# Kernel optimization log

Measured on AMD Instinct MI355X. Metric: run time of the kernel, lower is better.

## Reference

```python
import jax, jax.numpy as jnp
import numpy as np

N = 50000      # nodes
E = 800000     # edges
F_IN = 9       # node features
H = 128        # model_units
G = 64         # graphs in batch


def _lin_init(key, fan_in, fan_out):
    k1, k2 = jax.random.split(key)
    lim = 1.0 / np.sqrt(fan_in)
    W = jax.random.uniform(k1, (fan_in, fan_out), minval=-lim, maxval=lim, dtype=jnp.float32)
    b = jax.random.uniform(k2, (fan_out,), minval=-lim, maxval=lim, dtype=jnp.float32)
    return W, b


def setup_inputs() -> dict:
    key = jax.random.key(0)
    ks = jax.random.split(key, 12)
    x = jax.random.normal(ks[0], (N, F_IN), dtype=jnp.float32)
    edge_index = jax.random.randint(ks[1], (2, E), 0, N, dtype=jnp.int32)
    batch = jnp.sort(jax.random.randint(ks[2], (N,), 0, G, dtype=jnp.int32))
    W1, b1 = _lin_init(ks[3], F_IN, H)      # conv1 (GCN)
    W2, b2 = _lin_init(ks[4], H, H)         # conv2 (GCN, shared across layers)
    We1, be1 = _lin_init(ks[5], 2 * H, H)   # EdgeConv MLP layer 1
    We2, be2 = _lin_init(ks[6], H, H)       # EdgeConv MLP layer 2
    Wf1, bf1 = _lin_init(ks[7], H, H)
    Wf2, bf2 = _lin_init(ks[8], H, 32)
    Wf3, bf3 = _lin_init(ks[9], 32, 1)
    return {"x": x, "edge_index": edge_index, "batch": batch,
            "W1": W1, "b1": b1, "W2": W2, "b2": b2,
            "We1": We1, "be1": be1, "We2": We2, "be2": be2,
            "Wf1": Wf1, "bf1": bf1, "Wf2": Wf2, "bf2": bf2,
            "Wf3": Wf3, "bf3": bf3}


def _gcn(x, W, b, src, dst, dis):
    # GCNConv with implicit self-loops and symmetric normalization.
    h = x @ W                                              # [N,H]
    msg = h[src] * dis[src, None]                          # gather + scale
    agg = jax.ops.segment_sum(msg, dst, num_segments=N)    # scatter-add
    return dis[:, None] * agg + h * (dis * dis)[:, None] + b


def _edgeconv(x, We1, be1, We2, be2, src, dst):
    # EdgeConv: max_j MLP([x_i, x_j - x_i]) over incoming edges j->i.
    xi = x[dst]                                            # [E,H]
    xj = x[src]
    m = jnp.concatenate([xi, xj - xi], axis=-1)            # [E,2H]
    m = jax.nn.relu(m @ We1 + be1) @ We2 + be2             # [E,H]
    agg = jax.ops.segment_max(m, dst, num_segments=N)
    return jnp.where(jnp.isfinite(agg), agg, 0.0)          # isolated nodes -> 0


def reference(x, edge_index, batch, W1, b1, W2, b2, We1, be1, We2, be2,
              Wf1, bf1, Wf2, bf2, Wf3, bf3):
    src, dst = edge_index[0], edge_index[1]
    # degree (with self loop) for GCN normalization
    deg = jax.ops.segment_sum(jnp.ones((E,), jnp.float32), dst, num_segments=N) + 1.0
    dis = jax.lax.rsqrt(deg)

    h = jnp.tanh(_gcn(x, W1, b1, src, dst, dis))
    h = jnp.tanh(_edgeconv(h, We1, be1, We2, be2, src, dst))
    # model_layers = 3 -> loop body once, then final block (dropout = identity, eval)
    for _ in range(2):
        h = jnp.tanh(_gcn(h, W2, b2, src, dst, dis))
        h = jnp.tanh(_edgeconv(h, We1, be1, We2, be2, src, dst))

    h = jnp.tanh(h @ Wf1 + bf1)
    h = jnp.tanh(h @ Wf2 + bf2)
    h = h @ Wf3 + bf3                                      # [N,1]

    counts = jax.ops.segment_sum(jnp.ones((N,), jnp.float32), batch, num_segments=G)
    pooled = jax.ops.segment_sum(h, batch, num_segments=G) / jnp.maximum(counts, 1.0)[:, None]
    return jax.nn.sigmoid(pooled)                          # [G,1]
```

## Files before the change

### kernel.cpp

```cpp
#include <hip/hip_runtime.h>
#include <hip/hip_bf16.h>

#define N_NODES 50000
#define N_EDGES 800000
#define F_IN 9
#define H 128
#define G_GRAPHS 64
#define HH (H * H)
#define MAXT (N_EDGES / 16 + N_NODES)

typedef short bf16x8 __attribute__((ext_vector_type(8)));
typedef float f32x4 __attribute__((ext_vector_type(4)));
typedef float f32x2 __attribute__((ext_vector_type(2)));

static __device__ inline short f2b(float f) {
    __hip_bfloat16 h = __float2bfloat16(f);
    return *reinterpret_cast<short*>(&h);
}
static __device__ inline float blo(unsigned u) { return __uint_as_float(u << 16); }
static __device__ inline float bhi(unsigned u) { return __uint_as_float(u & 0xFFFF0000u); }
static __device__ inline f32x2 up2(unsigned u) {
    f32x2 r; r.x = __uint_as_float(u << 16); r.y = __uint_as_float(u); return r;
}
static __device__ inline unsigned encodef(float f) {
    unsigned u = __float_as_uint(f);
    return (u & 0x80000000u) ? ~u : (u | 0x80000000u);
}
static __device__ inline float decodef(unsigned u) {
    return __uint_as_float((u & 0x80000000u) ? (u ^ 0x80000000u) : ~u);
}
static __device__ inline unsigned cvtpk(float lo, float hi) {
    unsigned r;
    asm("v_cvt_pk_bf16_f32 %0, %1, %2" : "=v"(r) : "v"(lo), "v"(hi));
    return r;
}

__global__ __launch_bounds__(256) void k_detect(const unsigned* __restrict__ x, int* flag,
                                                float* pooled, float* counts) {
    __shared__ int cnt;
    if (threadIdx.x == 0) cnt = 0;
    __syncthreads();
    unsigned u = x[threadIdx.x];
    int e = (u >> 7) & 0xFF;
    if (e >= 0x70 && e <= 0x83) atomicAdd(&cnt, 1);
    if (threadIdx.x < G_GRAPHS) { pooled[threadIdx.x] = 0.f; counts[threadIdx.x] = 0.f; }
    __syncthreads();
    if (threadIdx.x == 0) *flag = (cnt >= 128) ? 1 : 0;
}

struct CvtArgs { const void* src[15]; float* dst[15]; };

__global__ __launch_bounds__(256) void k_cvt_all(CvtArgs a, const int* __restrict__ flag) {
    const int sz[15] = {450000, 1152, 128, 16384, 128, 32768, 128, 16384, 128,
                        16384, 128, 4096, 32, 32, 1};
    int i = blockIdx.x * 256 + threadIdx.x;
    int fl = *flag;
    int base = 0;
    #pragma unroll
    for (int s = 0; s < 15; ++s) {
        if (i >= base && i < base + sz[s]) {
            int off = i - base;
            float v = fl ? __bfloat162float(((const __hip_bfloat16*)a.src[s])[off])
                         : ((const float*)a.src[s])[off];
            a.dst[s][off] = v;
        }
        base += sz[s];
    }
}

__global__ __launch_bounds__(256) void k_zero(float* p, int n) {
    int i = blockIdx.x * 256 + threadIdx.x;
    if (i < n) p[i] = 0.f;
}

__global__ __launch_bounds__(256) void k_prep_all(const float* __restrict__ We1,
                                                  const float* __restrict__ W2,
                                                  const float* __restrict__ Wf1,
                                                  const float* __restrict__ Wf2,
                                                  const float* __restrict__ We2,
                                                  short* WfU, short* WfV, short* WfW2,
                                                  short* WfF1, short* WfF2, short* We2f) {
    int b = blockIdx.x;
    const float* W; const float* Wm = nullptr; short* out; int NT = 8; int tid;
    if (b < 8)       { W = We1;      Wm = We1 + HH; out = WfU;  tid = b * 256 + threadIdx.x; }
    else if (b < 16) { W = We1 + HH; out = WfV;  tid = (b - 8) * 256 + threadIdx.x; }
    else if (b < 24) { W = W2;       out = WfW2; tid = (b - 16) * 256 + threadIdx.x; }
    else if (b < 32) { W = Wf1;      out = WfF1; tid = (b - 24) * 256 + threadIdx.x; }
    else if (b < 40) { W = We2;      out = We2f; tid = (b - 32) * 256 + threadIdx.x; }
    else             { W = Wf2;      out = WfF2; NT = 2; tid = (b - 40) * 256 + threadIdx.x; }
    int total = 4 * NT * 64;
    if (tid >= total) return;
    int kc = tid / (NT * 64);
    int ct = (tid / 64) % NT;
    int lane = tid & 63;
    int Nc = NT * 16;
    int kb = kc * 32 + (lane >> 4) * 8;
    int col = ct * 16 + (lane & 15);
    #pragma unroll
    for (int j = 0; j < 8; ++j) {
        float w = W[(kb + j) * Nc + col];
        if (Wm) w -= Wm[(kb + j) * Nc + col];
        out[tid * 8 + j] = f2b(w);
    }
}

__global__ __launch_bounds__(256) void k_hist(const int* __restrict__ dst, int* cnt) {
    int e = blockIdx.x * 256 + threadIdx.x;
    if (e < N_EDGES) atomicAdd(&cnt[dst[e]], 1);
}

__global__ __launch_bounds__(256) void k_scan1d(const int* __restrict__ deg,
                                                int* __restrict__ outA, int* __restrict__ outB,
                                                int* __restrict__ bsA, int* __restrict__ bsB) {
    __shared__ int ldsA[256], ldsB[256];
    int base = blockIdx.x * 2048;
    int t = threadIdx.x;
    int localA[8], localB[8];
    int sA = 0, sB = 0;
    #pragma unroll
    for (int j = 0; j < 8; ++j) {
        int idx = base + t * 8 + j;
        int v = (idx < N_NODES) ? deg[idx] : 0;
        int tc = (v + 15) >> 4;
        localA[j] = sA; sA += v;
        localB[j] = sB; sB += tc;
    }
    ldsA[t] = sA; ldsB[t] = sB;
    __syncthreads();
    if (t == 0) {
        int run = 0;
        for (int i = 0; i < 256; ++i) { int v = ldsA[i]; ldsA[i] = run; run += v; }
        bsA[blockIdx.x] = run;
        run = 0;
        for (int i = 0; i < 256; ++i) { int v = ldsB[i]; ldsB[i] = run; run += v; }
        bsB[blockIdx.x] = run;
    }
    __syncthreads();
    int oA = ldsA[t], oB = ldsB[t];
    #pragma unroll
    for (int j = 0; j < 8; ++j) {
        int idx = base + t * 8 + j;
        if (idx < N_NODES) { outA[idx] = oA + localA[j]; outB[idx] = oB + localB[j]; }
    }
}

__global__ void k_scan2d(int* bsA, int* bsB, int nb, int* rowptr, int* tstart, int* ntiles) {
    int run = 0;
    for (int i = 0; i < nb; ++i) { int v = bsA[i]; bsA[i] = run; run += v; }
    rowptr[N_NODES] = N_EDGES;
    run = 0;
    for (int i = 0; i < nb; ++i) { int v = bsB[i]; bsB[i] = run; run += v; }
    tstart[N_NODES] = run;
    *ntiles = run;
}

__global__ __launch_bounds__(256) void k_scan3d(int* rowptr, int* tstart,
                                                const int* __restrict__ bsA,
                                                const int* __restrict__ bsB) {
    int idx = blockIdx.x * 256 + threadIdx.x;
    if (idx < N_NODES) {
        rowptr[idx] += bsA[idx >> 11];
        tstart[idx] += bsB[idx >> 11];
    }
}

__global__ __launch_bounds__(256) void k_scatter(const int* __restrict__ src, const int* __restrict__ dst,
                                                 const int* __restrict__ rowptr, int* cursor,
                                                 int* __restrict__ csr_src) {
    int e = blockIdx.x * 256 + threadIdx.x;
    if (e >= N_EDGES) return;
    int d = dst[e];
    int pos = rowptr[d] + atomicSub(&cursor[d], 1) - 1;
    csr_src[pos] = src[e];
}

__global__ __launch_bounds__(256) void k_dis_counts(const int* __restrict__ rowptr, float* dis,
                                                    const int* __restrict__ batch, float* counts) {
    __shared__ float lc[G_GRAPHS];
    if (threadIdx.x < G_GRAPHS) lc[threadIdx.x] = 0.f;
    __syncthreads();
    int n = blockIdx.x * 256 + threadIdx.x;
    if (n < N_NODES) {
        int deg = rowptr[n + 1] - rowptr[n];
        dis[n] = rsqrtf((float)deg + 1.0f);
        atomicAdd(&lc[batch[n]], 1.0f);
    }
    __syncthreads();
    if (threadIdx.x < G_GRAPHS && lc[threadIdx.x] > 0.f)
        atomicAdd(&counts[threadIdx.x], lc[threadIdx.x]);
}

__global__ __launch_bounds__(256) void k_tfill(const int* __restrict__ rowptr,
                                               const int* __restrict__ csr_src,
                                               const int* __restrict__ tstart,
                                               int* __restrict__ tileN,
                                               int* __restrict__ tileSrc) {
    int n = blockIdx.x * 256 + threadIdx.x;
    if (n >= N_NODES) return;
    int t0 = tstart[n], t1 = tstart[n + 1];
    int beg = rowptr[n], end = rowptr[n + 1];
    for (int t = t0; t < t1; ++t) {
        tileN[t] = n;
        int tb = beg + (t - t0) * 16;
        #pragma unroll 4
        for (int j = 0; j < 16; ++j) {
            int ei = tb + j;
            tileSrc[t * 16 + j] = csr_src[ei < end ? ei : end - 1];
        }
    }
}

__global__ __launch_bounds__(256) void k_gemm_f32bf_scale(const float* __restrict__ A,
                                                          const float* __restrict__ W,
                                                          const float* __restrict__ dis,
                                                          short* __restrict__ out, int M) {
    __shared__ float w_lds[F_IN * H];
    for (int i = threadIdx.x; i < F_IN * H; i += 256) w_lds[i] = W[i];
    __syncthreads();
    int row = blockIdx.x * 8 + threadIdx.x / 32;
    int c4 = (threadIdx.x & 31) << 2;
    if (row >= M) return;
    const float* a = A + (size_t)row * F_IN;
    float acc0 = 0.f, acc1 = 0.f, acc2 = 0.f, acc3 = 0.f;
    #pragma unroll
    for (int k = 0; k < F_IN; ++k) {
        float av = a[k];
        float4 w = *reinterpret_cast<const float4*>(&w_lds[k * H + c4]);
        acc0 = fmaf(av, w.x, acc0);
        acc1 = fmaf(av, w.y, acc1);
        acc2 = fmaf(av, w.z, acc2);
        acc3 = fmaf(av, w.w, acc3);
    }
    float dv = dis[row];
    uint2 o = make_uint2(cvtpk(acc0 * dv, acc1 * dv), cvtpk(acc2 * dv, acc3 * dv));
    *reinterpret_cast<uint2*>(&out[(size_t)row * H + c4]) = o;
}

__global__ __launch_bounds__(512) void k_gemm_dual(const short* __restrict__ A,
                                                   const short* __restrict__ WfU,
                                                   const short* __restrict__ WfV,
                                                   const float* __restrict__ be1,
                                                   short* __restrict__ U,
                                                   short* __restrict__ V,
                                                   unsigned* __restrict__ aggEnc, int M) {
    __shared__ short wl[32768];
    for (int i = threadIdx.x * 8; i < 16384; i += 4096) {
        *reinterpret_cast<f32x4*>(&wl[i])         = *reinterpret_cast<const f32x4*>(&WfU[i]);
        *reinterpret_cast<f32x4*>(&wl[16384 + i]) = *reinterpret_cast<const f32x4*>(&WfV[i]);
    }
    {
        int r0 = blockIdx.x * 128;
        uint4* base = reinterpret_cast<uint4*>(aggEnc + (size_t)r0 * H);
        const uint4 z = make_uint4(0, 0, 0, 0);
        #pragma unroll
        for (int i = 0; i < 8; ++i) {
            int idx = threadIdx.x + i * 512;
            int row = r0 + (idx >> 5);
            if (row < M) base[idx] = z;
        }
    }
    __syncthreads();
    int wv = threadIdx.x >> 6, lane = threadIdx.x & 63;
    int er = lane & 15, kg = lane >> 4;
    int row0 = (blockIdx.x * 8 + wv) * 16;
    if (row0 >= M) return;
    bf16x8 af[4];
    #pragma unroll
    for (int kc = 0; kc < 4; ++kc)
        af[kc] = *reinterpret_cast<const bf16x8*>(&A[(size_t)(row0 + er) * H + kc * 32 + kg * 8]);
    const f32x4 vzero = {0.f, 0.f, 0.f, 0.f};
    f32x4 acc[8];
    #pragma unroll
    for (int ct = 0; ct < 8; ++ct) acc[ct] = vzero;
    #pragma unroll
    for (int kc = 0; kc < 4; ++kc)
        #pragma unroll
        for (int ct = 0; ct < 8; ++ct) {
            bf16x8 bf = *reinterpret_cast<const bf16x8*>(&wl[((kc * 8 + ct) * 64 + lane) * 8]);
            acc[ct] = __builtin_amdgcn_mfma_f32_16x16x32_bf16(af[kc], bf, acc[ct], 0, 0, 0);
        }
    #pragma unroll
    for (int ct = 0; ct < 8; ++ct) {
        int col = ct * 16 + er;
        float bv = be1[col];
        #pragma unroll
        for (int r = 0; r < 4; ++r)
            U[(size_t)(row0 + kg * 4 + r) * H + col] = f2b(acc[ct][r] + bv);
    }
    #pragma unroll
    for (int ct = 0; ct < 8; ++ct) acc[ct] = vzero;
    #pragma unroll
    for (int kc = 0; kc < 4; ++kc)
        #pragma unroll
        for (int ct = 0; ct < 8; ++ct) {
            bf16x8 bf = *reinterpret_cast<const bf16x8*>(&wl[16384 + ((kc * 8 + ct) * 64 + lane) * 8]);
            acc[ct] = __builtin_amdgcn_mfma_f32_16x16x32_bf16(af[kc], bf, acc[ct], 0, 0, 0);
        }
    #pragma unroll
    for (int ct = 0; ct < 8; ++ct) {
        int col = ct * 16 + er;
        #pragma unroll
        for (int r = 0; r < 4; ++r)
            V[(size_t)(row0 + kg * 4 + r) * H + col] = f2b(acc[ct][r]);
    }
}

__global__ __launch_bounds__(512) void k_gemm_scale_agg(const unsigned* __restrict__ aggEnc,
                                                        const float* __restrict__ be2,
                                                        const short* __restrict__ Wf,
                                                        const float* __restrict__ dis,
                                                        short* __restrict__ out, int M) {
    __shared__ short wl[16384];
    for (int i = threadIdx.x * 8; i < 16384; i += 4096)
        *reinterpret_cast<f32x4*>(&wl[i]) = *reinterpret_cast<const f32x4*>(&Wf[i]);
    __syncthreads();
    int wv = threadIdx.x >> 6, lane = threadIdx.x & 63;
    int er = lane & 15, kg = lane >> 4;
    int row0 = (blockIdx.x * 8 + wv) * 16;
    if (row0 >= M) return;
    bf16x8 af[4];
    #pragma unroll
    for (int kc = 0; kc < 4; ++kc) {
        int basec = kc * 32 + kg * 8;
        const unsigned* ap = &aggEnc[(size_t)(row0 + er) * H + basec];
        uint4 q0 = *reinterpret_cast<const uint4*>(ap);
        uint4 q1 = *reinterpret_cast<const uint4*>(ap + 4);
        float f0 = q0.x ? tanhf(decodef(q0.x) + be2[basec + 0]) : 0.f;
        float f1 = q0.y ? tanhf(decodef(q0.y) + be2[basec + 1]) : 0.f;
        float f2 = q0.z ? tanhf(decodef(q0.z) + be2[basec + 2]) : 0.f;
        float f3 = q0.w ? tanhf(decodef(q0.w) + be2[basec + 3]) : 0.f;
        float f4 = q1.x ? tanhf(decodef(q1.x) + be2[basec + 4]) : 0.f;
        float f5 = q1.y ? tanhf(decodef(q1.y) + be2[basec + 5]) : 0.f;
        float f6 = q1.z ? tanhf(decodef(q1.z) + be2[basec + 6]) : 0.f;
        float f7 = q1.w ? tanhf(decodef(q1.w) + be2[basec + 7]) : 0.f;
        union { unsigned u[4]; bf16x8 v; } A;
        A.u[0] = cvtpk(f0, f1); A.u[1] = cvtpk(f2, f3);
        A.u[2] = cvtpk(f4, f5); A.u[3] = cvtpk(f6, f7);
        af[kc] = A.v;
    }
    const f32x4 vzero = {0.f, 0.f, 0.f, 0.f};
    f32x4 acc[8];
    #pragma unroll
    for (int ct = 0; ct < 8; ++ct) acc[ct] = vzero;
    #pragma unroll
    for (int kc = 0; kc < 4; ++kc)
        #pragma unroll
        for (int ct = 0; ct < 8; ++ct) {
            bf16x8 bf = *reinterpret_cast<const bf16x8*>(&wl[((kc * 8 + ct) * 64 + lane) * 8]);
            acc[ct] = __builtin_amdgcn_mfma_f32_16x16x32_bf16(af[kc], bf, acc[ct], 0, 0, 0);
        }
    float dv[4];
    #pragma unroll
    for (int r = 0; r < 4; ++r) dv[r] = dis[row0 + kg * 4 + r];
    #pragma unroll
    for (int ct = 0; ct < 8; ++ct) {
        int col = ct * 16 + er;
        #pragma unroll
        for (int r = 0; r < 4; ++r)
            out[(size_t)(row0 + kg * 4 + r) * H + col] = f2b(acc[ct][r] * dv[r]);
    }
}

__global__ __launch_bounds__(256) void k_gcn_fused(const int* __restrict__ rowptr,
                                                   const int* __restrict__ csr_src,
                                                   const short* __restrict__ hWs,
                                                   const float* __restrict__ dis,
                                                   const float* __restrict__ bias,
                                                   short* __restrict__ out) {
    int wv = threadIdx.x >> 6, lane = threadIdx.x & 63;
    const unsigned* hw = (const unsigned*)hWs;
    const f32x2 z2 = {0.f, 0.f};
    for (int n = blockIdx.x * 4 + wv; n < N_NODES; n += gridDim.x * 4) {
        int beg = rowptr[n], end = rowptr[n + 1];
        f32x2 sa = z2, sb = z2, sc = z2, sd = z2;
        int e = beg;
        for (; e + 8 <= end; e += 8) {
            int s0 = csr_src[e],     s1 = csr_src[e + 1], s2 = csr_src[e + 2], s3 = csr_src[e + 3];
            int s4 = csr_src[e + 4], s5 = csr_src[e + 5], s6 = csr_src[e + 6], s7 = csr_src[e + 7];
            unsigned w0 = hw[(size_t)s0 * 64 + lane];
            unsigned w1 = hw[(size_t)s1 * 64 + lane];
            unsigned w2 = hw[(size_t)s2 * 64 + lane];
            unsigned w3 = hw[(size_t)s3 * 64 + lane];
            unsigned w4 = hw[(size_t)s4 * 64 + lane];
            unsigned w5 = hw[(size_t)s5 * 64 + lane];
            unsigned w6 = hw[(size_t)s6 * 64 + lane];
            unsigned w7 = hw[(size_t)s7 * 64 + lane];
            sa += up2(w0); sb += up2(w1); sc += up2(w2); sd += up2(w3);
            sa += up2(w4); sb += up2(w5); sc += up2(w6); sd += up2(w7);
        }
        for (; e + 4 <= end; e += 4) {
            int s0 = csr_src[e], s1 = csr_src[e + 1], s2 = csr_src[e + 2], s3 = csr_src[e + 3];
            unsigned w0 = hw[(size_t)s0 * 64 + lane];
            unsigned w1 = hw[(size_t)s1 * 64 + lane];
            unsigned w2 = hw[(size_t)s2 * 64 + lane];
            unsigned w3 = hw[(size_t)s3 * 64 + lane];
            sa += up2(w0); sb += up2(w1); sc += up2(w2); sd += up2(w3);
        }
        for (; e < end; ++e) sa += up2(hw[(size_t)csr_src[e] * 64 + lane]);
        f32x2 s = (sa + sb) + (sc + sd);
        float dn = dis[n];
        f32x2 wn2 = up2(hw[(size_t)n * 64 + lane]);
        float r0 = tanhf(dn * (s.x + wn2.x) + bias[lane * 2]);
        float r1 = tanhf(dn * (s.y + wn2.y) + bias[lane * 2 + 1]);
        *reinterpret_cast<unsigned*>(&out[(size_t)n * H + lane * 2]) = cvtpk(r0, r1);
    }
}

__global__ __launch_bounds__(512) void k_edge_tile(const int* __restrict__ tileN,
                                                   const int* __restrict__ tileSrc,
                                                   const int* __restrict__ ntilesp,
                                                   const short* __restrict__ U,
                                                   const short* __restrict__ V,
                                                   const short* __restrict__ We2f,
                                                   unsigned* aggEnc) {
    int nt = *ntilesp;
    if ((int)(blockIdx.x * 8) >= nt) return;
    __shared__ short wl[16384];
    for (int i = threadIdx.x * 8; i < 16384; i += 4096)
        *reinterpret_cast<f32x4*>(&wl[i]) = *reinterpret_cast<const f32x4*>(&We2f[i]);
    __syncthreads();
    int wv = threadIdx.x >> 6, lane = threadIdx.x & 63;
    int er = lane & 15, kg = lane >> 4, kseg = kg * 8;
    int tid = blockIdx.x * 8 + wv;
    if (tid >= nt) return;
    int n = tileN[tid];
    int s = tileSrc[tid * 16 + er];
    const f32x4 vzero = {0.f, 0.f, 0.f, 0.f};
    const f32x2 z2 = {0.f, 0.f};
    f32x4 acc[8];
    #pragma unroll
    for (int ct = 0; ct < 8; ++ct) acc[ct] = vzero;
    #pragma unroll
    for (int kc = 0; kc < 4; ++kc) {
        uint4 uu4 = *reinterpret_cast<const uint4*>(&U[(size_t)n * H + kc * 32 + kseg]);
        uint4 vv4 = *reinterpret_cast<const uint4*>(&V[(size_t)s * H + kc * 32 + kseg]);
        union { unsigned u[4]; bf16x8 v; } A;
        f32x2 t;
        t = __builtin_elementwise_max(up2(uu4.x) + up2(vv4.x), z2); A.u[0] = cvtpk(t.x, t.y);
        t = __builtin_elementwise_max(up2(uu4.y) + up2(vv4.y), z2); A.u[1] = cvtpk(t.x, t.y);
        t = __builtin_elementwise_max(up2(uu4.z) + up2(vv4.z), z2); A.u[2] = cvtpk(t.x, t.y);
        t = __builtin_elementwise_max(up2(uu4.w) + up2(vv4.w), z2); A.u[3] = cvtpk(t.x, t.y);
        #pragma unroll
        for (int ct = 0; ct < 8; ++ct) {
            bf16x8 bf = *reinterpret_cast<const bf16x8*>(&wl[((kc * 8 + ct) * 64 + lane) * 8]);
            acc[ct] = __builtin_amdgcn_mfma_f32_16x16x32_bf16(A.v, bf, acc[ct], 0, 0, 0);
        }
    }
    float cm[8];
    #pragma unroll
    for (int ct = 0; ct < 8; ++ct) {
        float v = fmaxf(fmaxf(fmaxf(acc[ct][0], acc[ct][1]), acc[ct][2]), acc[ct][3]);
        v = fmaxf(v, __shfl_xor(v, 16));
        v = fmaxf(v, __shfl_xor(v, 32));
        cm[ct] = v;
    }
    float vA, vB;
    if (kg == 0)      { vA = cm[0]; vB = cm[1]; }
    else if (kg == 1) { vA = cm[2]; vB = cm[3]; }
    else if (kg == 2) { vA = cm[4]; vB = cm[5]; }
    else              { vA = cm[6]; vB = cm[7]; }
    int colA = (kg * 2) * 16 + er;
    int colB = (kg * 2 + 1) * 16 + er;
    atomicMax(&aggEnc[(size_t)n * H + colA], encodef(vA));
    atomicMax(&aggEnc[(size_t)n * H + colB], encodef(vB));
}

__global__ __launch_bounds__(512) void k_final_mlp_agg(const unsigned* __restrict__ aggEnc,
                                                       const float* __restrict__ be2,
                                                       const short* __restrict__ WfF1,
                                                       const short* __restrict__ WfF2,
                                                       const float* __restrict__ bf1,
                                                       const float* __restrict__ bf2,
                                                       const float* __restrict__ Wf3,
                                                       const float* __restrict__ bf3,
                                                       const int* __restrict__ batch,
                                                       float* pooled, int M) {
    __shared__ short wl1[16384];
    __shared__ short wl2[4096];
    __shared__ short tb[8][2048];
    __shared__ float lp[G_GRAPHS];
    for (int i = threadIdx.x * 8; i < 16384; i += 4096)
        *reinterpret_cast<f32x4*>(&wl1[i]) = *reinterpret_cast<const f32x4*>(&WfF1[i]);
    {
        int i = threadIdx.x * 8;
        if (i < 4096)
            *reinterpret_cast<f32x4*>(&wl2[i]) = *reinterpret_cast<const f32x4*>(&WfF2[i]);
    }
    if (threadIdx.x < G_GRAPHS) lp[threadIdx.x] = 0.f;
    __syncthreads();
    int wv = threadIdx.x >> 6, lane = threadIdx.x & 63;
    int er = lane & 15, kg = lane >> 4;
    int row0 = (blockIdx.x * 8 + wv) * 16;
    bool active = row0 < M;
    const f32x4 vzero = {0.f, 0.f, 0.f, 0.f};
    if (active) {
        bf16x8 af[4];
        #pragma unroll
        for (int kc = 0; kc < 4; ++kc) {
            int basec = kc * 32 + kg * 8;
            const unsigned* ap = &aggEnc[(size_t)(row0 + er) * H + basec];
            uint4 q0 = *reinterpret_cast<const uint4*>(ap);
            uint4 q1 = *reinterpret_cast<const uint4*>(ap + 4);
            float f0 = q0.x ? tanhf(decodef(q0.x) + be2[basec + 0]) : 0.f;
            float f1 = q0.y ? tanhf(decodef(q0.y) + be2[basec + 1]) : 0.f;
            float f2 = q0.z ? tanhf(decodef(q0.z) + be2[basec + 2]) : 0.f;
            float f3 = q0.w ? tanhf(decodef(q0.w) + be2[basec + 3]) : 0.f;
            float f4 = q1.x ? tanhf(decodef(q1.x) + be2[basec + 4]) : 0.f;
            float f5 = q1.y ? tanhf(decodef(q1.y) + be2[basec + 5]) : 0.f;
            float f6 = q1.z ? tanhf(decodef(q1.z) + be2[basec + 6]) : 0.f;
            float f7 = q1.w ? tanhf(decodef(q1.w) + be2[basec + 7]) : 0.f;
            union { unsigned u[4]; bf16x8 v; } A;
            A.u[0] = cvtpk(f0, f1); A.u[1] = cvtpk(f2, f3);
            A.u[2] = cvtpk(f4, f5); A.u[3] = cvtpk(f6, f7);
            af[kc] = A.v;
        }
        f32x4 acc[8];
        #pragma unroll
        for (int ct = 0; ct < 8; ++ct) acc[ct] = vzero;
        #pragma unroll
        for (int kc = 0; kc < 4; ++kc)
            #pragma unroll
            for (int ct = 0; ct < 8; ++ct) {
                bf16x8 bf = *reinterpret_cast<const bf16x8*>(&wl1[((kc * 8 + ct) * 64 + lane) * 8]);
                acc[ct] = __builtin_amdgcn_mfma_f32_16x16x32_bf16(af[kc], bf, acc[ct], 0, 0, 0);
            }
        #pragma unroll
        for (int ct = 0; ct < 8; ++ct) {
            int col = ct * 16 + er;
            float bv = bf1[col];
            #pragma unroll
            for (int r = 0; r < 4; ++r)
                tb[wv][(kg * 4 + r) * 128 + col] = f2b(tanhf(acc[ct][r] + bv));
        }
    }
    __syncthreads();
    if (active) {
        bf16x8 af2[4];
        #pragma unroll
        for (int kc = 0; kc < 4; ++kc)
            af2[kc] = *reinterpret_cast<const bf16x8*>(&tb[wv][er * 128 + kc * 32 + kg * 8]);
        f32x4 a2[2];
        a2[0] = vzero; a2[1] = vzero;
        #pragma unroll
        for (int kc = 0; kc < 4; ++kc)
            #pragma unroll
            for (int ct = 0; ct < 2; ++ct) {
                bf16x8 bf = *reinterpret_cast<const bf16x8*>(&wl2[((kc * 2 + ct) * 64 + lane) * 8]);
                a2[ct] = __builtin_amdgcn_mfma_f32_16x16x32_bf16(af2[kc], bf, a2[ct], 0, 0, 0);
            }
        float w3a = Wf3[er], w3b = Wf3[16 + er];
        float b2a = bf2[er], b2b = bf2[16 + er];
        float bf3v = bf3[0];
        float psum[4];
        #pragma unroll
        for (int r = 0; r < 4; ++r) {
            float f2a = tanhf(a2[0][r] + b2a);
            float f2c = tanhf(a2[1][r] + b2b);
            float p = f2a * w3a + f2c * w3b;
            p += __shfl_xor(p, 1);
            p += __shfl_xor(p, 2);
            p += __shfl_xor(p, 4);
            p += __shfl_xor(p, 8);
            psum[r] = p + bf3v;
        }
        if (er == 0) {
            #pragma unroll
            for (int r = 0; r < 4; ++r) {
                int n = row0 + kg * 4 + r;
                if (n < M) atomicAdd(&lp[batch[n]], psum[r]);
            }
        }
    }
    __syncthreads();
    if (threadIdx.x < G_GRAPHS && lp[threadIdx.x] != 0.f)
        atomicAdd(&pooled[threadIdx.x], lp[threadIdx.x]);
}

__global__ __launch_bounds__(64) void k_final(const float* pooled, const float* counts,
                                              void* out, const int* __restrict__ flag) {
    int g = threadIdx.x;
    if (g < G_GRAPHS) {
        float v = pooled[g] / fmaxf(counts[g], 1.0f);
        float s = 1.0f / (1.0f + expf(-v));
        if (*flag) ((__hip_bfloat16*)out)[g] = __float2bfloat16(s);
        else       ((float*)out)[g] = s;
    }
}

extern "C" void kernel_launch(void* const* d_in, const int* in_sizes, int n_in,
                              void* d_out, int out_size, void* d_ws, size_t ws_size,
                              hipStream_t stream) {
    const int* ei    = (const int*)d_in[1];
    const int* src   = ei;
    const int* dst   = ei + N_EDGES;
    const int* batch = (const int*)d_in[2];

    float* ws = (float*)d_ws;
    size_t off = 0;
    auto alloc = [&](size_t n) { off = (off + 3) & ~(size_t)3; float* p = ws + off; off += n; return p; };

    const size_t NH = (size_t)N_NODES * H;
    short* hb     = (short*)alloc(NH / 2);
    short* Ub     = (short*)alloc(NH / 2);
    short* Vb     = (short*)alloc(NH / 2);
    unsigned* aggEnc = (unsigned*)alloc(NH);
    float* xf     = alloc((size_t)N_NODES * F_IN);
    float* dis    = alloc(N_NODES);
    float* pooled = alloc(G_GRAPHS);
    float* counts = alloc(G_GRAPHS);
    int*   flag   = (int*)alloc(1);
    int*   rowptr = (int*)alloc(N_NODES + 1);
    int*   cursor = (int*)alloc(N_NODES);
    int*   csrsrc = (int*)alloc(N_EDGES);
    int*   bsums  = (int*)alloc(32);
    int*   bsums2 = (int*)alloc(32);
    int*   tstart = (int*)alloc(N_NODES + 1);
    int*   ntiles = (int*)alloc(1);
    int*   tileN  = (int*)alloc(MAXT);
    int*   tileSrc= (int*)alloc((size_t)MAXT * 16);

    float* W1  = alloc(F_IN * H);
    float* b1  = alloc(H);
    float* W2  = alloc(HH);
    float* b2  = alloc(H);
    float* We1 = alloc(2 * HH);
    float* be1 = alloc(H);
    float* We2 = alloc(HH);
    float* be2 = alloc(H);
    float* Wf1 = alloc(HH);
    float* bf1 = alloc(H);
    float* Wf2 = alloc(H * 32);
    float* bf2 = alloc(32);
    float* Wf3 = alloc(32);
    float* bf3 = alloc(4);
    short* WfU  = (short*)alloc(8192);
    short* WfV  = (short*)alloc(8192);
    short* WfW2 = (short*)alloc(8192);
    short* WfF1 = (short*)alloc(8192);
    short* WfF2 = (short*)alloc(2048);
    short* We2f = (short*)alloc(8192);

    const int eB    = (N_EDGES + 255) / 256;
    const int nB    = (N_NODES + 255) / 256;
    const int scanB = (N_NODES + 2047) / 2048;
    const int mfmaB = (N_NODES / 16 + 7) / 8;
    const int gcnB  = (N_NODES + 3) / 4;
    const int tileB = (MAXT + 7) / 8;

    k_detect<<<1, 256, 0, stream>>>((const unsigned*)d_in[0], flag, pooled, counts);

    CvtArgs ca;
    const int srcIdx[15] = {0, 3, 4, 5, 6, 7, 8, 9, 10, 11, 12, 13, 14, 15, 16};
    float* dsts[15] = {xf, W1, b1, W2, b2, We1, be1, We2, be2, Wf1, bf1, Wf2, bf2, Wf3, bf3};
    for (int s = 0; s < 15; ++s) { ca.src[s] = d_in[srcIdx[s]]; ca.dst[s] = dsts[s]; }
    const int cvtTotal = 450000 + 1152 + 128 + 16384 + 128 + 32768 + 128 + 16384 + 128
                       + 16384 + 128 + 4096 + 32 + 32 + 1;
    k_cvt_all<<<(cvtTotal + 255) / 256, 256, 0, stream>>>(ca, flag);

    k_prep_all<<<42, 256, 0, stream>>>(We1, W2, Wf1, Wf2, We2,
                                       WfU, WfV, WfW2, WfF1, WfF2, We2f);

    k_zero<<<nB, 256, 0, stream>>>((float*)cursor, N_NODES);
    k_hist<<<eB, 256, 0, stream>>>(dst, cursor);
    k_scan1d<<<scanB, 256, 0, stream>>>(cursor, rowptr, tstart, bsums, bsums2);
    k_scan2d<<<1, 1, 0, stream>>>(bsums, bsums2, scanB, rowptr, tstart, ntiles);
    k_scan3d<<<nB, 256, 0, stream>>>(rowptr, tstart, bsums, bsums2);
    k_scatter<<<eB, 256, 0, stream>>>(src, dst, rowptr, cursor, csrsrc);
    k_dis_counts<<<nB, 256, 0, stream>>>(rowptr, dis, batch, counts);
    k_tfill<<<nB, 256, 0, stream>>>(rowptr, csrsrc, tstart, tileN, tileSrc);

    k_gemm_f32bf_scale<<<(N_NODES + 7) / 8, 256, 0, stream>>>(xf, W1, dis, Ub, N_NODES);
    k_gcn_fused<<<gcnB, 256, 0, stream>>>(rowptr, csrsrc, Ub, dis, b1, hb);

    for (int iter = 0; iter < 3; ++iter) {
        k_gemm_dual<<<mfmaB, 512, 0, stream>>>(hb, WfU, WfV, be1, Ub, Vb, aggEnc, N_NODES);
        k_edge_tile<<<tileB, 512, 0, stream>>>(tileN, tileSrc, ntiles, Ub, Vb, We2f, aggEnc);
        if (iter < 2) {
            k_gemm_scale_agg<<<mfmaB, 512, 0, stream>>>(aggEnc, be2, WfW2, dis, Ub, N_NODES);
            k_gcn_fused<<<gcnB, 256, 0, stream>>>(rowptr, csrsrc, Ub, dis, b2, hb);
        }
    }

    k_final_mlp_agg<<<mfmaB, 512, 0, stream>>>(aggEnc, be2, WfF1, WfF2, bf1, bf2, Wf3, bf3,
                                               batch, pooled, N_NODES);
    k_final<<<1, 64, 0, stream>>>(pooled, counts, d_out, flag);
}
```

Measured before the change: 501.3 us.

## Fuse preprocessing kernels and make edge-tile kernel persistent

Zeroing of the cursor array is folded into the conversion kernel, and degree normalization plus per-graph counts move into the scan kernel. The scatter kernel now writes tile source indices directly, so the old tile-fill pass shrinks to a padding kernel. The edge-tile MLP kernel becomes a grid-stride persistent kernel with 1024 blocks, loading the weight matrix into LDS once per block instead of once per 8 tiles. The goal is to cut launch count and repeated LDS weight loads, at the cost of a fixed grid size that may underfill or serialize work.

```diff
diff --git a/kernel.cpp b/kernel.cpp
--- a/kernel.cpp
+++ b/kernel.cpp
@@ -18,7 +18,6 @@
     return *reinterpret_cast<short*>(&h);
 }
 static __device__ inline float blo(unsigned u) { return __uint_as_float(u << 16); }
-static __device__ inline float bhi(unsigned u) { return __uint_as_float(u & 0xFFFF0000u); }
 static __device__ inline f32x2 up2(unsigned u) {
     f32x2 r; r.x = __uint_as_float(u << 16); r.y = __uint_as_float(u); return r;
 }
@@ -50,10 +49,17 @@
 
 struct CvtArgs { const void* src[15]; float* dst[15]; };
 
-__global__ __launch_bounds__(256) void k_cvt_all(CvtArgs a, const int* __restrict__ flag) {
+__global__ __launch_bounds__(256) void k_cvt_all(CvtArgs a, const int* __restrict__ flag,
+                                                 int* __restrict__ cursor) {
     const int sz[15] = {450000, 1152, 128, 16384, 128, 32768, 128, 16384, 128,
                         16384, 128, 4096, 32, 32, 1};
+    const int cvtTotal = 537873;
     int i = blockIdx.x * 256 + threadIdx.x;
+    if (i >= cvtTotal) {
+        int c = i - cvtTotal;
+        if (c < N_NODES) cursor[c] = 0;
+        return;
+    }
     int fl = *flag;
     int base = 0;
     #pragma unroll
@@ -66,11 +72,6 @@
         }
         base += sz[s];
     }
-}
-
-__global__ __launch_bounds__(256) void k_zero(float* p, int n) {
-    int i = blockIdx.x * 256 + threadIdx.x;
-    if (i < n) p[i] = 0.f;
 }
 
 __global__ __launch_bounds__(256) void k_prep_all(const float* __restrict__ We1,
@@ -111,8 +112,13 @@
 
 __global__ __launch_bounds__(256) void k_scan1d(const int* __restrict__ deg,
                                                 int* __restrict__ outA, int* __restrict__ outB,
-                                                int* __restrict__ bsA, int* __restrict__ bsB) {
+                                                int* __restrict__ bsA, int* __restrict__ bsB,
+                                                float* __restrict__ dis,
+                                                const int* __restrict__ batch,
+                                                float* __restrict__ counts) {
     __shared__ int ldsA[256], ldsB[256];
+    __shared__ float lc[G_GRAPHS];
+    if (threadIdx.x < G_GRAPHS) lc[threadIdx.x] = 0.f;
     int base = blockIdx.x * 2048;
     int t = threadIdx.x;
     int localA[8], localB[8];
@@ -124,6 +130,10 @@
         int tc = (v + 15) >> 4;
         localA[j] = sA; sA += v;
         localB[j] = sB; sB += tc;
+        if (idx < N_NODES) {
+            dis[idx] = rsqrtf((float)v + 1.0f);
+            atomicAdd(&lc[batch[idx]], 1.0f);
+        }
     }
     ldsA[t] = sA; ldsB[t] = sB;
     __syncthreads();
@@ -142,6 +152,8 @@
         int idx = base + t * 8 + j;
         if (idx < N_NODES) { outA[idx] = oA + localA[j]; outB[idx] = oB + localB[j]; }
     }
+    if (threadIdx.x < G_GRAPHS && lc[threadIdx.x] > 0.f)
+        atomicAdd(&counts[threadIdx.x], lc[threadIdx.x]);
 }
 
 __global__ void k_scan2d(int* bsA, int* bsB, int nb, int* rowptr, int* tstart, int* ntiles) {
@@ -165,48 +177,36 @@
 }
 
 __global__ __launch_bounds__(256) void k_scatter(const int* __restrict__ src, const int* __restrict__ dst,
-                                                 const int* __restrict__ rowptr, int* cursor,
-                                                 int* __restrict__ csr_src) {
+                                                 const int* __restrict__ rowptr,
+                                                 const int* __restrict__ tstart,
+                                                 int* cursor,
+                                                 int* __restrict__ csr_src,
+                                                 int* __restrict__ tileSrc) {
     int e = blockIdx.x * 256 + threadIdx.x;
     if (e >= N_EDGES) return;
     int d = dst[e];
-    int pos = rowptr[d] + atomicSub(&cursor[d], 1) - 1;
-    csr_src[pos] = src[e];
-}
-
-__global__ __launch_bounds__(256) void k_dis_counts(const int* __restrict__ rowptr, float* dis,
-                                                    const int* __restrict__ batch, float* counts) {
-    __shared__ float lc[G_GRAPHS];
-    if (threadIdx.x < G_GRAPHS) lc[threadIdx.x] = 0.f;
-    __syncthreads();
-    int n = blockIdx.x * 256 + threadIdx.x;
-    if (n < N_NODES) {
-        int deg = rowptr[n + 1] - rowptr[n];
-        dis[n] = rsqrtf((float)deg + 1.0f);
-        atomicAdd(&lc[batch[n]], 1.0f);
-    }
-    __syncthreads();
-    if (threadIdx.x < G_GRAPHS && lc[threadIdx.x] > 0.f)
-        atomicAdd(&counts[threadIdx.x], lc[threadIdx.x]);
-}
-
-__global__ __launch_bounds__(256) void k_tfill(const int* __restrict__ rowptr,
-                                               const int* __restrict__ csr_src,
-                                               const int* __restrict__ tstart,
-                                               int* __restrict__ tileN,
-                                               int* __restrict__ tileSrc) {
+    int sv = src[e];
+    int local = atomicSub(&cursor[d], 1) - 1;
+    csr_src[rowptr[d] + local] = sv;
+    tileSrc[(tstart[d] + (local >> 4)) * 16 + (local & 15)] = sv;
+}
+
+__global__ __launch_bounds__(256) void k_tpad(const int* __restrict__ rowptr,
+                                              const int* __restrict__ csr_src,
+                                              const int* __restrict__ tstart,
+                                              int* __restrict__ tileN,
+                                              int* __restrict__ tileSrc) {
     int n = blockIdx.x * 256 + threadIdx.x;
     if (n >= N_NODES) return;
     int t0 = tstart[n], t1 = tstart[n + 1];
-    int beg = rowptr[n], end = rowptr[n + 1];
-    for (int t = t0; t < t1; ++t) {
-        tileN[t] = n;
-        int tb = beg + (t - t0) * 16;
-        #pragma unroll 4
-        for (int j = 0; j < 16; ++j) {
-            int ei = tb + j;
-            tileSrc[t * 16 + j] = csr_src[ei < end ? ei : end - 1];
-        }
+    if (t0 == t1) return;
+    for (int t = t0; t < t1; ++t) tileN[t] = n;
+    int deg = rowptr[n + 1] - rowptr[n];
+    int rem = deg & 15;
+    if (rem) {
+        int lastS = csr_src[rowptr[n + 1] - 1];
+        int tb = (t1 - 1) * 16;
+        for (int j = rem; j < 16; ++j) tileSrc[tb + j] = lastS;
     }
 }
 
@@ -333,10 +333,10 @@
         float f5 = q1.y ? tanhf(decodef(q1.y) + be2[basec + 5]) : 0.f;
         float f6 = q1.z ? tanhf(decodef(q1.z) + be2[basec + 6]) : 0.f;
         float f7 = q1.w ? tanhf(decodef(q1.w) + be2[basec + 7]) : 0.f;
-        union { unsigned u[4]; bf16x8 v; } A;
-        A.u[0] = cvtpk(f0, f1); A.u[1] = cvtpk(f2, f3);
-        A.u[2] = cvtpk(f4, f5); A.u[3] = cvtpk(f6, f7);
-        af[kc] = A.v;
+        union { unsigned u[4]; bf16x8 v; } Afr;
+        Afr.u[0] = cvtpk(f0, f1); Afr.u[1] = cvtpk(f2, f3);
+        Afr.u[2] = cvtpk(f4, f5); Afr.u[3] = cvtpk(f6, f7);
+        af[kc] = Afr.v;
     }
     const f32x4 vzero = {0.f, 0.f, 0.f, 0.f};
     f32x4 acc[8];
@@ -413,56 +413,55 @@
                                                    const short* __restrict__ V,
                                                    const short* __restrict__ We2f,
                                                    unsigned* aggEnc) {
-    int nt = *ntilesp;
-    if ((int)(blockIdx.x * 8) >= nt) return;
     __shared__ short wl[16384];
     for (int i = threadIdx.x * 8; i < 16384; i += 4096)
         *reinterpret_cast<f32x4*>(&wl[i]) = *reinterpret_cast<const f32x4*>(&We2f[i]);
     __syncthreads();
+    int nt = *ntilesp;
     int wv = threadIdx.x >> 6, lane = threadIdx.x & 63;
     int er = lane & 15, kg = lane >> 4, kseg = kg * 8;
-    int tid = blockIdx.x * 8 + wv;
-    if (tid >= nt) return;
-    int n = tileN[tid];
-    int s = tileSrc[tid * 16 + er];
     const f32x4 vzero = {0.f, 0.f, 0.f, 0.f};
     const f32x2 z2 = {0.f, 0.f};
-    f32x4 acc[8];
-    #pragma unroll
-    for (int ct = 0; ct < 8; ++ct) acc[ct] = vzero;
-    #pragma unroll
-    for (int kc = 0; kc < 4; ++kc) {
-        uint4 uu4 = *reinterpret_cast<const uint4*>(&U[(size_t)n * H + kc * 32 + kseg]);
-        uint4 vv4 = *reinterpret_cast<const uint4*>(&V[(size_t)s * H + kc * 32 + kseg]);
-        union { unsigned u[4]; bf16x8 v; } A;
-        f32x2 t;
-        t = __builtin_elementwise_max(up2(uu4.x) + up2(vv4.x), z2); A.u[0] = cvtpk(t.x, t.y);
-        t = __builtin_elementwise_max(up2(uu4.y) + up2(vv4.y), z2); A.u[1] = cvtpk(t.x, t.y);
-        t = __builtin_elementwise_max(up2(uu4.z) + up2(vv4.z), z2); A.u[2] = cvtpk(t.x, t.y);
-        t = __builtin_elementwise_max(up2(uu4.w) + up2(vv4.w), z2); A.u[3] = cvtpk(t.x, t.y);
+    for (int tid = blockIdx.x * 8 + wv; tid < nt; tid += gridDim.x * 8) {
+        int n = tileN[tid];
+        int s = tileSrc[tid * 16 + er];
+        f32x4 acc[8];
+        #pragma unroll
+        for (int ct = 0; ct < 8; ++ct) acc[ct] = vzero;
+        #pragma unroll
+        for (int kc = 0; kc < 4; ++kc) {
+            uint4 uu4 = *reinterpret_cast<const uint4*>(&U[(size_t)n * H + kc * 32 + kseg]);
+            uint4 vv4 = *reinterpret_cast<const uint4*>(&V[(size_t)s * H + kc * 32 + kseg]);
+            union { unsigned u[4]; bf16x8 v; } A;
+            f32x2 t;
+            t = __builtin_elementwise_max(up2(uu4.x) + up2(vv4.x), z2); A.u[0] = cvtpk(t.x, t.y);
+            t = __builtin_elementwise_max(up2(uu4.y) + up2(vv4.y), z2); A.u[1] = cvtpk(t.x, t.y);
+            t = __builtin_elementwise_max(up2(uu4.z) + up2(vv4.z), z2); A.u[2] = cvtpk(t.x, t.y);
+            t = __builtin_elementwise_max(up2(uu4.w) + up2(vv4.w), z2); A.u[3] = cvtpk(t.x, t.y);
+            #pragma unroll
+            for (int ct = 0; ct < 8; ++ct) {
+                bf16x8 bf = *reinterpret_cast<const bf16x8*>(&wl[((kc * 8 + ct) * 64 + lane) * 8]);
+                acc[ct] = __builtin_amdgcn_mfma_f32_16x16x32_bf16(A.v, bf, acc[ct], 0, 0, 0);
+            }
+        }
+        float cm[8];
         #pragma unroll
         for (int ct = 0; ct < 8; ++ct) {
-            bf16x8 bf = *reinterpret_cast<const bf16x8*>(&wl[((kc * 8 + ct) * 64 + lane) * 8]);
-            acc[ct] = __builtin_amdgcn_mfma_f32_16x16x32_bf16(A.v, bf, acc[ct], 0, 0, 0);
-        }
-    }
-    float cm[8];
-    #pragma unroll
-    for (int ct = 0; ct < 8; ++ct) {
-        float v = fmaxf(fmaxf(fmaxf(acc[ct][0], acc[ct][1]), acc[ct][2]), acc[ct][3]);
-        v = fmaxf(v, __shfl_xor(v, 16));
-        v = fmaxf(v, __shfl_xor(v, 32));
-        cm[ct] = v;
-    }
-    float vA, vB;
-    if (kg == 0)      { vA = cm[0]; vB = cm[1]; }
-    else if (kg == 1) { vA = cm[2]; vB = cm[3]; }
-    else if (kg == 2) { vA = cm[4]; vB = cm[5]; }
-    else              { vA = cm[6]; vB = cm[7]; }
-    int colA = (kg * 2) * 16 + er;
-    int colB = (kg * 2 + 1) * 16 + er;
-    atomicMax(&aggEnc[(size_t)n * H + colA], encodef(vA));
-    atomicMax(&aggEnc[(size_t)n * H + colB], encodef(vB));
+            float v = fmaxf(fmaxf(fmaxf(acc[ct][0], acc[ct][1]), acc[ct][2]), acc[ct][3]);
+            v = fmaxf(v, __shfl_xor(v, 16));
+            v = fmaxf(v, __shfl_xor(v, 32));
+            cm[ct] = v;
+        }
+        float vA, vB;
+        if (kg == 0)      { vA = cm[0]; vB = cm[1]; }
+        else if (kg == 1) { vA = cm[2]; vB = cm[3]; }
+        else if (kg == 2) { vA = cm[4]; vB = cm[5]; }
+        else              { vA = cm[6]; vB = cm[7]; }
+        int colA = (kg * 2) * 16 + er;
+        int colB = (kg * 2 + 1) * 16 + er;
+        atomicMax(&aggEnc[(size_t)n * H + colA], encodef(vA));
+        atomicMax(&aggEnc[(size_t)n * H + colB], encodef(vB));
+    }
 }
 
 __global__ __launch_bounds__(512) void k_final_mlp_agg(const unsigned* __restrict__ aggEnc,
@@ -645,7 +644,7 @@
     const int scanB = (N_NODES + 2047) / 2048;
     const int mfmaB = (N_NODES / 16 + 7) / 8;
     const int gcnB  = (N_NODES + 3) / 4;
-    const int tileB = (MAXT + 7) / 8;
+    const int edgeB = 1024;
 
     k_detect<<<1, 256, 0, stream>>>((const unsigned*)d_in[0], flag, pooled, counts);
 
@@ -653,28 +652,26 @@
     const int srcIdx[15] = {0, 3, 4, 5, 6, 7, 8, 9, 10, 11, 12, 13, 14, 15, 16};
     float* dsts[15] = {xf, W1, b1, W2, b2, We1, be1, We2, be2, Wf1, bf1, Wf2, bf2, Wf3, bf3};
     for (int s = 0; s < 15; ++s) { ca.src[s] = d_in[srcIdx[s]]; ca.dst[s] = dsts[s]; }
-    const int cvtTotal = 450000 + 1152 + 128 + 16384 + 128 + 32768 + 128 + 16384 + 128
-                       + 16384 + 128 + 4096 + 32 + 32 + 1;
-    k_cvt_all<<<(cvtTotal + 255) / 256, 256, 0, stream>>>(ca, flag);
+    const int cvtTotal = 537873 + N_NODES;
+    k_cvt_all<<<(cvtTotal + 255) / 256, 256, 0, stream>>>(ca, flag, cursor);
 
     k_prep_all<<<42, 256, 0, stream>>>(We1, W2, Wf1, Wf2, We2,
                                        WfU, WfV, WfW2, WfF1, WfF2, We2f);
 
-    k_zero<<<nB, 256, 0, stream>>>((float*)cursor, N_NODES);
     k_hist<<<eB, 256, 0, stream>>>(dst, cursor);
-    k_scan1d<<<scanB, 256, 0, stream>>>(cursor, rowptr, tstart, bsums, bsums2);
+    k_scan1d<<<scanB, 256, 0, stream>>>(cursor, rowptr, tstart, bsums, bsums2,
+                                        dis, batch, counts);
     k_scan2d<<<1, 1, 0, stream>>>(bsums, bsums2, scanB, rowptr, tstart, ntiles);
     k_scan3d<<<nB, 256, 0, stream>>>(rowptr, tstart, bsums, bsums2);
-    k_scatter<<<eB, 256, 0, stream>>>(src, dst, rowptr, cursor, csrsrc);
-    k_dis_counts<<<nB, 256, 0, stream>>>(rowptr, dis, batch, counts);
-    k_tfill<<<nB, 256, 0, stream>>>(rowptr, csrsrc, tstart, tileN, tileSrc);
+    k_scatter<<<eB, 256, 0, stream>>>(src, dst, rowptr, tstart, cursor, csrsrc, tileSrc);
+    k_tpad<<<nB, 256, 0, stream>>>(rowptr, csrsrc, tstart, tileN, tileSrc);
 
     k_gemm_f32bf_scale<<<(N_NODES + 7) / 8, 256, 0, stream>>>(xf, W1, dis, Ub, N_NODES);
     k_gcn_fused<<<gcnB, 256, 0, stream>>>(rowptr, csrsrc, Ub, dis, b1, hb);
 
     for (int iter = 0; iter < 3; ++iter) {
         k_gemm_dual<<<mfmaB, 512, 0, stream>>>(hb, WfU, WfV, be1, Ub, Vb, aggEnc, N_NODES);
-        k_edge_tile<<<tileB, 512, 0, stream>>>(tileN, tileSrc, ntiles, Ub, Vb, We2f, aggEnc);
+        k_edge_tile<<<edgeB, 512, 0, stream>>>(tileN, tileSrc, ntiles, Ub, Vb, We2f, aggEnc);
         if (iter < 2) {
             k_gemm_scale_agg<<<mfmaB, 512, 0, stream>>>(aggEnc, be2, WfW2, dis, Ub, N_NODES);
             k_gcn_fused<<<gcnB, 256, 0, stream>>>(rowptr, csrsrc, Ub, dis, b2, hb);
```

Result: faster. 480.8 us (-4.1%).
